# Optimization experiments

Hardware: AMD Instinct MI355X
Metric: run time of the kernel (lower is better)

The kernel has to match this reference:

```python
import jax, jax.numpy as jnp
import numpy as np

N = 100000
E = 1600000
DIM = 128
HID = 16
HEADS = 4
NUM_CLASSES = 2
NEG_SLOPE = 0.2


def _glorot(key, shape):
    fan_in, fan_out = shape[0], shape[-1]
    lim = jnp.sqrt(6.0 / (fan_in + fan_out))
    return jax.random.uniform(key, shape, jnp.float32, -lim, lim)


def setup_inputs() -> dict:
    key = jax.random.key(0)
    ks = jax.random.split(key, 12)
    x = jax.random.normal(ks[0], (N, DIM), jnp.float32)
    edge_index = jax.random.randint(ks[1], (2, E), 0, N, jnp.int32)
    # conv1: in=DIM, out=HID, heads=HEADS
    W1 = _glorot(ks[2], (DIM, HEADS * HID))
    att_src1 = _glorot(ks[3], (HEADS, HID))
    att_dst1 = _glorot(ks[4], (HEADS, HID))
    b1 = jnp.zeros((HEADS * HID,), jnp.float32)
    # conv2: in=HEADS*HID, out=NUM_CLASSES, heads=1
    W2 = _glorot(ks[5], (HEADS * HID, NUM_CLASSES))
    att_src2 = _glorot(ks[6], (1, NUM_CLASSES))
    att_dst2 = _glorot(ks[7], (1, NUM_CLASSES))
    b2 = jnp.zeros((NUM_CLASSES,), jnp.float32)
    return {"x": x, "edge_index": edge_index, "W1": W1, "att_src1": att_src1,
            "att_dst1": att_dst1, "b1": b1, "W2": W2, "att_src2": att_src2,
            "att_dst2": att_dst2, "b2": b2}


def gat_conv(x, src, dst, W, a_src, a_dst, bias, heads, out_ch):
    n = x.shape[0]
    h = (x @ W).reshape(n, heads, out_ch)                      # [N,H,C]
    alpha_s = jnp.sum(h * a_src[None], axis=-1)                # [N,H]
    alpha_d = jnp.sum(h * a_dst[None], axis=-1)                # [N,H]
    e = alpha_s[src] + alpha_d[dst]                            # [Etot,H]
    e = jnp.where(e > 0, e, NEG_SLOPE * e)                     # leaky_relu
    m = jax.ops.segment_max(e, dst, num_segments=n)            # segment softmax
    e = jnp.exp(e - m[dst])
    s = jax.ops.segment_sum(e, dst, num_segments=n)
    alpha = e / (s[dst] + 1e-16)                               # [Etot,H]
    msg = h[src] * alpha[..., None]                            # [Etot,H,C]
    out = jax.ops.segment_sum(msg, dst, num_segments=n)        # [N,H,C]
    return out.reshape(n, heads * out_ch) + bias


def reference(x, edge_index, W1, att_src1, att_dst1, b1, W2, att_src2, att_dst2, b2):
    n = x.shape[0]
    loops = jnp.arange(n, dtype=edge_index.dtype)
    src = jnp.concatenate([edge_index[0], loops])
    dst = jnp.concatenate([edge_index[1], loops])
    # dropout p=0.6 is identity in eval mode
    h = gat_conv(x, src, dst, W1, att_src1, att_dst1, b1, HEADS, HID)
    h = jax.nn.elu(h)
    out = gat_conv(h, src, dst, W2, att_src2, att_dst2, b2, 1, NUM_CLASSES)
    return out
```

## Files before the change

### kernel.cpp

```cpp
#include <hip/hip_runtime.h>
#include <math.h>


#define NB 256
#define BSH 9
#define SRC_MASK 0x1FFFF
#define KC_CHUNK 2048
#define KC_PT 8
#define MAXB 9216

static __device__ __forceinline__ unsigned short f2bf(float f) {
    union { float f; unsigned int u; } v; v.f = f;
    unsigned int r = (v.u + 0x7fffu + ((v.u >> 16) & 1u)) >> 16;
    return (unsigned short)r;
}
static __device__ __forceinline__ float bf2f(unsigned short s) {
    union { unsigned int u; float f; } v; v.u = ((unsigned int)s) << 16;
    return v.f;
}
static __device__ __forceinline__ float lrexp(float raw) {
    return __expf(raw > 0.f ? raw : 0.2f * raw);
}

__global__ __launch_bounds__(256) void k_gemm1(const float* __restrict__ x,
                                               const float* __restrict__ W,
                                               const float* __restrict__ att_s,
                                               const float* __restrict__ att_d,
                                               unsigned short* __restrict__ h1b,
                                               float* __restrict__ as1,
                                               float* __restrict__ ad1,
                                               int* __restrict__ bcursor, int n) {
    __shared__ float xs[64 * 132];
    __shared__ float Ws[128 * 64];
    const int t = threadIdx.x;
    const int row0 = blockIdx.x * 64;
    if (blockIdx.x == 0) bcursor[t] = 0;
    for (int i = t; i < 2048; i += 256)
        ((float4*)Ws)[i] = ((const float4*)W)[i];
    for (int i = t; i < 2048; i += 256) {
        int r = i >> 5, k4 = i & 31;
        float4 v = make_float4(0.f, 0.f, 0.f, 0.f);
        if (row0 + r < n) v = ((const float4*)x)[(size_t)(row0 + r) * 32 + k4];
        *(float4*)&xs[r * 132 + k4 * 4] = v;
    }
    __syncthreads();
    const int tx = t & 15, ty = t >> 4;
    float acc[4][4] = {};
    for (int k = 0; k < 128; k += 4) {
        float4 av[4], bv[4];
#pragma unroll
        for (int i = 0; i < 4; ++i) av[i] = *(const float4*)&xs[(ty * 4 + i) * 132 + k];
#pragma unroll
        for (int kk = 0; kk < 4; ++kk) bv[kk] = *(const float4*)&Ws[(k + kk) * 64 + tx * 4];
#pragma unroll
        for (int kk = 0; kk < 4; ++kk) {
            float4 b = bv[kk];
#pragma unroll
            for (int i = 0; i < 4; ++i) {
                float a = ((const float*)&av[i])[kk];
                acc[i][0] += a * b.x; acc[i][1] += a * b.y;
                acc[i][2] += a * b.z; acc[i][3] += a * b.w;
            }
        }
    }
    float4 sv = ((const float4*)att_s)[tx];
    float4 dv = ((const float4*)att_d)[tx];
    float ps[4], pd[4];
#pragma unroll
    for (int i = 0; i < 4; ++i) {
        ps[i] = acc[i][0] * sv.x + acc[i][1] * sv.y + acc[i][2] * sv.z + acc[i][3] * sv.w;
        pd[i] = acc[i][0] * dv.x + acc[i][1] * dv.y + acc[i][2] * dv.z + acc[i][3] * dv.w;
        int r = row0 + ty * 4 + i;
        if (r < n) {
            ushort4 b;
            b.x = f2bf(acc[i][0]); b.y = f2bf(acc[i][1]);
            b.z = f2bf(acc[i][2]); b.w = f2bf(acc[i][3]);
            ((ushort4*)h1b)[(size_t)r * 16 + tx] = b;
        }
    }
    __syncthreads();
    float* redA = xs;
    float* redB = xs + 1024;
#pragma unroll
    for (int i = 0; i < 4; ++i) {
        int row = ty * 4 + i;
        redA[row * 16 + tx] = ps[i];
        redB[row * 16 + tx] = pd[i];
    }
    __syncthreads();
    {
        int row = t >> 2, h = t & 3;
        int r = row0 + row;
        if (r < n) {
            const float* pa = &redA[row * 16 + h * 4];
            const float* pb = &redB[row * 16 + h * 4];
            as1[r * 4 + h] = pa[0] + pa[1] + pa[2] + pa[3];
            ad1[r * 4 + h] = pb[0] + pb[1] + pb[2] + pb[3];
        }
    }
}

__global__ __launch_bounds__(256) void kC_bin(const int* __restrict__ src,
                                              const int* __restrict__ dst,
                                              int* __restrict__ bcursor,
                                              unsigned int* __restrict__ staged, int E) {
    __shared__ unsigned int pairs[KC_CHUNK];
    __shared__ unsigned char binOf[KC_CHUNK];
    __shared__ int h[NB], lofs[NB], lcur[NB], gbase[NB];
    int t = threadIdx.x;
    int base = blockIdx.x * KC_CHUNK;
    int cnt = E - base; if (cnt > KC_CHUNK) cnt = KC_CHUNK;
    h[t] = 0; __syncthreads();
    unsigned int myV[KC_PT]; int myBin[KC_PT];
#pragma unroll
    for (int k = 0; k < KC_PT; ++k) {
        int li = k * 256 + t;
        myBin[k] = -1;
        if (li < cnt) {
            int gi = base + li;
            int s = src[gi], d = dst[gi];
            int bin = d >> BSH;
            myV[k] = ((unsigned int)(d & ((1 << BSH) - 1)) << 17) | (unsigned int)s;
            myBin[k] = bin;
            atomicAdd(&h[bin], 1);
        }
    }
    __syncthreads();
    int hv = h[t];
    lofs[t] = hv; __syncthreads();
    for (int o = 1; o < NB; o <<= 1) {
        int xv = (t >= o) ? lofs[t - o] : 0;
        __syncthreads();
        lofs[t] += xv; __syncthreads();
    }
    int excl = lofs[t] - hv;
    if (hv) gbase[t] = t * MAXB + atomicAdd(&bcursor[t], hv);
    __syncthreads();
    lofs[t] = excl; lcur[t] = excl;
    __syncthreads();
#pragma unroll
    for (int k = 0; k < KC_PT; ++k) {
        if (myBin[k] >= 0) {
            int p = atomicAdd(&lcur[myBin[k]], 1);
            pairs[p] = myV[k];
            binOf[p] = (unsigned char)myBin[k];
        }
    }
    __syncthreads();
    for (int i = t; i < cnt; i += 256) {
        int b = binOf[i];
        staged[gbase[b] + (i - lofs[b])] = pairs[i];
    }
}

__global__ __launch_bounds__(256) void kD_group(const unsigned int* __restrict__ staged,
                                                const int* __restrict__ bcursor,
                                                unsigned int* __restrict__ grouped,
                                                int* __restrict__ offs,
                                                int* __restrict__ dcnt, int n) {
    __shared__ int lh[512], lofs2[512], lcur2[512];
    __shared__ unsigned int st[MAXB];
    int t = threadIdx.x;
    int b = blockIdx.x;
    int base = b * MAXB;
    int cnt = bcursor[b];
    lh[t] = 0; lh[t + 256] = 0;
    __syncthreads();
    for (int i = t; i < cnt; i += 256)
        atomicAdd(&lh[staged[base + i] >> 17], 1);
    __syncthreads();
    int a0 = lh[2 * t], a1 = lh[2 * t + 1];
    int sp = a0 + a1;
    lcur2[t] = sp; __syncthreads();
    for (int o = 1; o < NB; o <<= 1) {
        int xv = (t >= o) ? lcur2[t - o] : 0;
        __syncthreads();
        lcur2[t] += xv; __syncthreads();
    }
    int excl = lcur2[t] - sp;
    lofs2[2 * t] = excl; lofs2[2 * t + 1] = excl + a0;
    __syncthreads();
#pragma unroll
    for (int q = 0; q < 2; ++q) {
        int dl = t + q * 256;
        int d = (b << BSH) + dl;
        if (d < n) {
            offs[d] = base + lofs2[dl];
            dcnt[d] = lh[dl];
        }
        lcur2[dl] = lofs2[dl];
    }
    __syncthreads();
    for (int i = t; i < cnt; i += 256) {
        unsigned int v = staged[base + i];
        int p = atomicAdd(&lcur2[v >> 17], 1);
        st[p] = v;
    }
    __syncthreads();
    for (int i = t; i < cnt; i += 256)
        grouped[base + i] = st[i];
}

__global__ __launch_bounds__(256) void k_agg1(
        const int* __restrict__ offs, const int* __restrict__ dcnt,
        const unsigned int* __restrict__ grouped,
        const unsigned short* __restrict__ h1b, const float* __restrict__ as1,
        const float* __restrict__ ad1, const float* __restrict__ b1,
        const float* __restrict__ W2,
        const float* __restrict__ att_s2, const float* __restrict__ att_d2,
        float4* __restrict__ pack, int n) {
    const int lane = threadIdx.x & 63;
    const int d = blockIdx.x * 4 + (threadIdx.x >> 6);
    if (d >= n) return;
    const int c = lane;
    const int h = lane >> 4;
    const int sub = lane & 15;
    const int off0 = offs[d];
    const int total = dcnt[d];
    const float adh = ad1[d * 4 + h];
    const float wselfv = lrexp(as1[d * 4 + h] + adh);

    float acc = wselfv * bf2f(h1b[(size_t)d * 64 + c]);
    float wsum = 0.f;

    int s_cur = d; float a_cur = 0.f; bool v_ok = (sub < total);
    if (v_ok) {
        unsigned int v = grouped[off0 + sub];
        s_cur = (int)(v & SRC_MASK);
        a_cur = as1[s_cur * 4 + h];
    }
    for (int base = 0; base < total; base += 16) {
        int en = base + 16 + sub;
        bool n_ok = (en < total);
        unsigned int v_n = 0;
        if (n_ok) v_n = grouped[off0 + en];

        float w = v_ok ? lrexp(a_cur + adh) : 0.f;
        wsum += w;
        int s = s_cur;
#pragma unroll
        for (int j = 0; j < 16; ++j) {
            int sj = __builtin_amdgcn_readlane(s, j);
            float wj = __shfl(w, (h << 4) + j);
            acc += wj * bf2f(h1b[(size_t)sj * 64 + c]);
        }
        int s_n = d; float a_n = 0.f;
        if (n_ok) {
            s_n = (int)(v_n & SRC_MASK);
            a_n = as1[s_n * 4 + h];
        }
        s_cur = s_n; a_cur = a_n; v_ok = n_ok;
    }
    wsum += __shfl_xor(wsum, 1);
    wsum += __shfl_xor(wsum, 2);
    wsum += __shfl_xor(wsum, 4);
    wsum += __shfl_xor(wsum, 8);
    wsum += wselfv;
    float o1 = acc / (wsum + 1e-16f) + b1[c];
    float o = o1 > 0.f ? o1 : (__expf(o1) - 1.f);
    float2 wv = ((const float2*)W2)[c];
    float p0 = o * wv.x, p1 = o * wv.y;
#pragma unroll
    for (int m = 1; m < 64; m <<= 1) {
        p0 += __shfl_xor(p0, m);
        p1 += __shfl_xor(p1, m);
    }
    if (lane == 0) {
        pack[d] = make_float4(p0, p1,
                              p0 * att_s2[0] + p1 * att_s2[1],
                              p0 * att_d2[0] + p1 * att_d2[1]);
    }
}

__global__ __launch_bounds__(256) void k_agg2(
        const int* __restrict__ offs, const int* __restrict__ dcnt,
        const unsigned int* __restrict__ grouped,
        const float4* __restrict__ pack, const float* __restrict__ b2,
        float* __restrict__ out, int n) {
    int t = threadIdx.x;
    int g = blockIdx.x * 16 + (t >> 4);
    int sub = t & 15;
    if (g >= n) return;
    int off0 = offs[g];
    int total = dcnt[g];
    float4 pg = pack[g];
    float ad = pg.w;
    float a0 = 0.f, a1 = 0.f, ws = 0.f;
    if (sub == 0) {
        float w = lrexp(pg.z + ad);
        a0 = w * pg.x; a1 = w * pg.y; ws = w;
    }
    for (int e = sub; e < total; e += 16) {
        int s = (int)(grouped[off0 + e] & SRC_MASK);
        float4 ps = pack[s];
        float w = lrexp(ps.z + ad);
        a0 += w * ps.x; a1 += w * ps.y; ws += w;
    }
#pragma unroll
    for (int m = 1; m < 16; m <<= 1) {
        a0 += __shfl_xor(a0, m);
        a1 += __shfl_xor(a1, m);
        ws += __shfl_xor(ws, m);
    }
    if (sub == 0) {
        float inv = 1.f / (ws + 1e-16f);
        out[(size_t)g * 2 + 0] = a0 * inv + b2[0];
        out[(size_t)g * 2 + 1] = a1 * inv + b2[1];
    }
}

extern "C" void kernel_launch(void* const* d_in, const int* in_sizes, int n_in,
                              void* d_out, int out_size, void* d_ws, size_t ws_size,
                              hipStream_t stream) {
    const float* x    = (const float*)d_in[0];
    const int*   ei   = (const int*)d_in[1];
    const float* W1   = (const float*)d_in[2];
    const float* as1w = (const float*)d_in[3];
    const float* ad1w = (const float*)d_in[4];
    const float* b1   = (const float*)d_in[5];
    const float* W2   = (const float*)d_in[6];
    const float* as2w = (const float*)d_in[7];
    const float* ad2w = (const float*)d_in[8];
    const float* b2   = (const float*)d_in[9];
    const int n = in_sizes[0] / 128;
    const int E = in_sizes[1] / 2;
    float* out = (float*)d_out;

    char* ws = (char*)d_ws;
    size_t off = 0;
    auto alloc = [&](size_t bytes) {
        void* p = ws + off;
        off = (off + bytes + 255) & ~(size_t)255;
        return p;
    };
    unsigned short* h1b = (unsigned short*)alloc((size_t)n * 64 * 2);
    float*  as1    = (float*)alloc((size_t)n * 4 * 4);
    float*  ad1    = (float*)alloc((size_t)n * 4 * 4);
    float4* pack   = (float4*)alloc((size_t)n * 16);
    int*    offs   = (int*)alloc((size_t)n * 4);
    int*    dcnt   = (int*)alloc((size_t)n * 4);
    int*    bcursor= (int*)alloc(NB * 4);
    unsigned int* staged  = (unsigned int*)alloc((size_t)NB * MAXB * 4);
    unsigned int* grouped = (unsigned int*)alloc((size_t)NB * MAXB * 4);

    const int nblk = (E + KC_CHUNK - 1) / KC_CHUNK;
    const int nbk = (n + 511) >> 9;
    k_gemm1<<<(n + 63) / 64, 256, 0, stream>>>(x, W1, as1w, ad1w, h1b, as1, ad1,
                                               bcursor, n);
    kC_bin<<<nblk, 256, 0, stream>>>(ei, ei + E, bcursor, staged, E);
    kD_group<<<nbk, 256, 0, stream>>>(staged, bcursor, grouped, offs, dcnt, n);
    k_agg1<<<(n + 3) / 4, 256, 0, stream>>>(offs, dcnt, grouped, h1b, as1, ad1,
                                            b1, W2, as2w, ad2w, pack, n);
    k_agg2<<<(n + 15) / 16, 256, 0, stream>>>(offs, dcnt, grouped, pack, b2, out, n);
}
```

Before: 241.0 us.

## Fuse GEMM and edge binning into one launch; per-lane row gather in agg1

Merges the layer-1 GEMM and the edge-binning pass into a single kernel whose blocks branch on blockIdx, and zeroes the bin cursors with a memset, so the two independent stages can overlap on the GPU. In k_agg1 each lane now loads a whole 16-element bf16 slice of one source row (two uint4 loads) and keeps 16 partial accumulators. A butterfly shuffle transpose then reduces these to per-channel values, replacing the 16-step readlane/shfl loop. The fused kernel uses a larger shared allocation (about 65 KB), which may reduce occupancy for the binning blocks.

```diff
diff --git a/kernel.cpp b/kernel.cpp
--- a/kernel.cpp
+++ b/kernel.cpp
@@ -14,142 +14,138 @@
     unsigned int r = (v.u + 0x7fffu + ((v.u >> 16) & 1u)) >> 16;
     return (unsigned short)r;
 }
-static __device__ __forceinline__ float bf2f(unsigned short s) {
-    union { unsigned int u; float f; } v; v.u = ((unsigned int)s) << 16;
-    return v.f;
-}
 static __device__ __forceinline__ float lrexp(float raw) {
     return __expf(raw > 0.f ? raw : 0.2f * raw);
 }
 
-__global__ __launch_bounds__(256) void k_gemm1(const float* __restrict__ x,
-                                               const float* __restrict__ W,
-                                               const float* __restrict__ att_s,
-                                               const float* __restrict__ att_d,
-                                               unsigned short* __restrict__ h1b,
-                                               float* __restrict__ as1,
-                                               float* __restrict__ ad1,
-                                               int* __restrict__ bcursor, int n) {
-    __shared__ float xs[64 * 132];
-    __shared__ float Ws[128 * 64];
+__global__ __launch_bounds__(256) void k_gemm_bin(
+        const float* __restrict__ x, const float* __restrict__ W,
+        const float* __restrict__ att_s, const float* __restrict__ att_d,
+        unsigned short* __restrict__ h1b, float* __restrict__ as1,
+        float* __restrict__ ad1,
+        const int* __restrict__ esrc, const int* __restrict__ edst,
+        int* __restrict__ bcursor, unsigned int* __restrict__ staged,
+        int nG, int E, int n) {
+    __shared__ __align__(16) char smem[66560];
     const int t = threadIdx.x;
-    const int row0 = blockIdx.x * 64;
-    if (blockIdx.x == 0) bcursor[t] = 0;
-    for (int i = t; i < 2048; i += 256)
-        ((float4*)Ws)[i] = ((const float4*)W)[i];
-    for (int i = t; i < 2048; i += 256) {
-        int r = i >> 5, k4 = i & 31;
-        float4 v = make_float4(0.f, 0.f, 0.f, 0.f);
-        if (row0 + r < n) v = ((const float4*)x)[(size_t)(row0 + r) * 32 + k4];
-        *(float4*)&xs[r * 132 + k4 * 4] = v;
-    }
-    __syncthreads();
-    const int tx = t & 15, ty = t >> 4;
-    float acc[4][4] = {};
-    for (int k = 0; k < 128; k += 4) {
-        float4 av[4], bv[4];
-#pragma unroll
-        for (int i = 0; i < 4; ++i) av[i] = *(const float4*)&xs[(ty * 4 + i) * 132 + k];
-#pragma unroll
-        for (int kk = 0; kk < 4; ++kk) bv[kk] = *(const float4*)&Ws[(k + kk) * 64 + tx * 4];
-#pragma unroll
-        for (int kk = 0; kk < 4; ++kk) {
-            float4 b = bv[kk];
-#pragma unroll
-            for (int i = 0; i < 4; ++i) {
-                float a = ((const float*)&av[i])[kk];
-                acc[i][0] += a * b.x; acc[i][1] += a * b.y;
-                acc[i][2] += a * b.z; acc[i][3] += a * b.w;
+
+    if (blockIdx.x < nG) {
+        float* xs = (float*)smem;
+        float* Ws = (float*)(smem + 33792);
+        const int row0 = blockIdx.x * 64;
+        for (int i = t; i < 2048; i += 256)
+            ((float4*)Ws)[i] = ((const float4*)W)[i];
+        for (int i = t; i < 2048; i += 256) {
+            int r = i >> 5, k4 = i & 31;
+            float4 v = make_float4(0.f, 0.f, 0.f, 0.f);
+            if (row0 + r < n) v = ((const float4*)x)[(size_t)(row0 + r) * 32 + k4];
+            *(float4*)&xs[r * 132 + k4 * 4] = v;
+        }
+        __syncthreads();
+        const int tx = t & 15, ty = t >> 4;
+        float acc[4][4] = {};
+        for (int k = 0; k < 128; k += 4) {
+            float4 av[4], bv[4];
+#pragma unroll
+            for (int i = 0; i < 4; ++i) av[i] = *(const float4*)&xs[(ty * 4 + i) * 132 + k];
+#pragma unroll
+            for (int kk = 0; kk < 4; ++kk) bv[kk] = *(const float4*)&Ws[(k + kk) * 64 + tx * 4];
+#pragma unroll
+            for (int kk = 0; kk < 4; ++kk) {
+                float4 b = bv[kk];
+#pragma unroll
+                for (int i = 0; i < 4; ++i) {
+                    float a = ((const float*)&av[i])[kk];
+                    acc[i][0] += a * b.x; acc[i][1] += a * b.y;
+                    acc[i][2] += a * b.z; acc[i][3] += a * b.w;
+                }
             }
         }
-    }
-    float4 sv = ((const float4*)att_s)[tx];
-    float4 dv = ((const float4*)att_d)[tx];
-    float ps[4], pd[4];
-#pragma unroll
-    for (int i = 0; i < 4; ++i) {
-        ps[i] = acc[i][0] * sv.x + acc[i][1] * sv.y + acc[i][2] * sv.z + acc[i][3] * sv.w;
-        pd[i] = acc[i][0] * dv.x + acc[i][1] * dv.y + acc[i][2] * dv.z + acc[i][3] * dv.w;
-        int r = row0 + ty * 4 + i;
-        if (r < n) {
-            ushort4 b;
-            b.x = f2bf(acc[i][0]); b.y = f2bf(acc[i][1]);
-            b.z = f2bf(acc[i][2]); b.w = f2bf(acc[i][3]);
-            ((ushort4*)h1b)[(size_t)r * 16 + tx] = b;
-        }
-    }
-    __syncthreads();
-    float* redA = xs;
-    float* redB = xs + 1024;
-#pragma unroll
-    for (int i = 0; i < 4; ++i) {
-        int row = ty * 4 + i;
-        redA[row * 16 + tx] = ps[i];
-        redB[row * 16 + tx] = pd[i];
-    }
-    __syncthreads();
-    {
-        int row = t >> 2, h = t & 3;
-        int r = row0 + row;
-        if (r < n) {
-            const float* pa = &redA[row * 16 + h * 4];
-            const float* pb = &redB[row * 16 + h * 4];
-            as1[r * 4 + h] = pa[0] + pa[1] + pa[2] + pa[3];
-            ad1[r * 4 + h] = pb[0] + pb[1] + pb[2] + pb[3];
-        }
-    }
-}
-
-__global__ __launch_bounds__(256) void kC_bin(const int* __restrict__ src,
-                                              const int* __restrict__ dst,
-                                              int* __restrict__ bcursor,
-                                              unsigned int* __restrict__ staged, int E) {
-    __shared__ unsigned int pairs[KC_CHUNK];
-    __shared__ unsigned char binOf[KC_CHUNK];
-    __shared__ int h[NB], lofs[NB], lcur[NB], gbase[NB];
-    int t = threadIdx.x;
-    int base = blockIdx.x * KC_CHUNK;
-    int cnt = E - base; if (cnt > KC_CHUNK) cnt = KC_CHUNK;
-    h[t] = 0; __syncthreads();
-    unsigned int myV[KC_PT]; int myBin[KC_PT];
-#pragma unroll
-    for (int k = 0; k < KC_PT; ++k) {
-        int li = k * 256 + t;
-        myBin[k] = -1;
-        if (li < cnt) {
-            int gi = base + li;
-            int s = src[gi], d = dst[gi];
-            int bin = d >> BSH;
-            myV[k] = ((unsigned int)(d & ((1 << BSH) - 1)) << 17) | (unsigned int)s;
-            myBin[k] = bin;
-            atomicAdd(&h[bin], 1);
-        }
-    }
-    __syncthreads();
-    int hv = h[t];
-    lofs[t] = hv; __syncthreads();
-    for (int o = 1; o < NB; o <<= 1) {
-        int xv = (t >= o) ? lofs[t - o] : 0;
-        __syncthreads();
-        lofs[t] += xv; __syncthreads();
-    }
-    int excl = lofs[t] - hv;
-    if (hv) gbase[t] = t * MAXB + atomicAdd(&bcursor[t], hv);
-    __syncthreads();
-    lofs[t] = excl; lcur[t] = excl;
-    __syncthreads();
-#pragma unroll
-    for (int k = 0; k < KC_PT; ++k) {
-        if (myBin[k] >= 0) {
-            int p = atomicAdd(&lcur[myBin[k]], 1);
-            pairs[p] = myV[k];
-            binOf[p] = (unsigned char)myBin[k];
-        }
-    }
-    __syncthreads();
-    for (int i = t; i < cnt; i += 256) {
-        int b = binOf[i];
-        staged[gbase[b] + (i - lofs[b])] = pairs[i];
+        float4 sv = ((const float4*)att_s)[tx];
+        float4 dv = ((const float4*)att_d)[tx];
+        float ps[4], pd[4];
+#pragma unroll
+        for (int i = 0; i < 4; ++i) {
+            ps[i] = acc[i][0] * sv.x + acc[i][1] * sv.y + acc[i][2] * sv.z + acc[i][3] * sv.w;
+            pd[i] = acc[i][0] * dv.x + acc[i][1] * dv.y + acc[i][2] * dv.z + acc[i][3] * dv.w;
+            int r = row0 + ty * 4 + i;
+            if (r < n) {
+                ushort4 b;
+                b.x = f2bf(acc[i][0]); b.y = f2bf(acc[i][1]);
+                b.z = f2bf(acc[i][2]); b.w = f2bf(acc[i][3]);
+                ((ushort4*)h1b)[(size_t)r * 16 + tx] = b;
+            }
+        }
+        __syncthreads();
+        float* redA = xs;
+        float* redB = xs + 1024;
+#pragma unroll
+        for (int i = 0; i < 4; ++i) {
+            int row = ty * 4 + i;
+            redA[row * 16 + tx] = ps[i];
+            redB[row * 16 + tx] = pd[i];
+        }
+        __syncthreads();
+        {
+            int row = t >> 2, h = t & 3;
+            int r = row0 + row;
+            if (r < n) {
+                const float* pa = &redA[row * 16 + h * 4];
+                const float* pb = &redB[row * 16 + h * 4];
+                as1[r * 4 + h] = pa[0] + pa[1] + pa[2] + pa[3];
+                ad1[r * 4 + h] = pb[0] + pb[1] + pb[2] + pb[3];
+            }
+        }
+    } else {
+        unsigned int* pairs = (unsigned int*)smem;
+        unsigned char* binOf = (unsigned char*)(smem + 8192);
+        int* hh    = (int*)(smem + 10240);
+        int* lofs  = (int*)(smem + 11264);
+        int* lcur  = (int*)(smem + 12288);
+        int* gbase = (int*)(smem + 13312);
+        int base = (blockIdx.x - nG) * KC_CHUNK;
+        int cnt = E - base; if (cnt > KC_CHUNK) cnt = KC_CHUNK;
+        hh[t] = 0; __syncthreads();
+        unsigned int myV[KC_PT]; int myBin[KC_PT];
+#pragma unroll
+        for (int k = 0; k < KC_PT; ++k) {
+            int li = k * 256 + t;
+            myBin[k] = -1;
+            if (li < cnt) {
+                int gi = base + li;
+                int s = esrc[gi], d = edst[gi];
+                int bin = d >> BSH;
+                myV[k] = ((unsigned int)(d & ((1 << BSH) - 1)) << 17) | (unsigned int)s;
+                myBin[k] = bin;
+                atomicAdd(&hh[bin], 1);
+            }
+        }
+        __syncthreads();
+        int hv = hh[t];
+        lofs[t] = hv; __syncthreads();
+        for (int o = 1; o < NB; o <<= 1) {
+            int xv = (t >= o) ? lofs[t - o] : 0;
+            __syncthreads();
+            lofs[t] += xv; __syncthreads();
+        }
+        int excl = lofs[t] - hv;
+        if (hv) gbase[t] = t * MAXB + atomicAdd(&bcursor[t], hv);
+        __syncthreads();
+        lofs[t] = excl; lcur[t] = excl;
+        __syncthreads();
+#pragma unroll
+        for (int k = 0; k < KC_PT; ++k) {
+            if (myBin[k] >= 0) {
+                int p = atomicAdd(&lcur[myBin[k]], 1);
+                pairs[p] = myV[k];
+                binOf[p] = (unsigned char)myBin[k];
+            }
+        }
+        __syncthreads();
+        for (int i = t; i < cnt; i += 256) {
+            int b = binOf[i];
+            staged[gbase[b] + (i - lofs[b])] = pairs[i];
+        }
     }
 }
 
@@ -212,53 +208,100 @@
     const int lane = threadIdx.x & 63;
     const int d = blockIdx.x * 4 + (threadIdx.x >> 6);
     if (d >= n) return;
-    const int c = lane;
-    const int h = lane >> 4;
+    const int q = lane >> 4;
     const int sub = lane & 15;
     const int off0 = offs[d];
     const int total = dcnt[d];
-    const float adh = ad1[d * 4 + h];
-    const float wselfv = lrexp(as1[d * 4 + h] + adh);
-
-    float acc = wselfv * bf2f(h1b[(size_t)d * 64 + c]);
+    const float adh = ad1[d * 4 + q];
+    const float wselfv = lrexp(as1[d * 4 + q] + adh);
+
+    float acc[16];
+#pragma unroll
+    for (int k = 0; k < 16; ++k) acc[k] = 0.f;
     float wsum = 0.f;
+
+    if (sub == 0) {
+        const uint4* rp = (const uint4*)(h1b + (size_t)d * 64 + q * 16);
+        uint4 ra = rp[0], rb = rp[1];
+        const unsigned int* ua = (const unsigned int*)&ra;
+        const unsigned int* ub = (const unsigned int*)&rb;
+#pragma unroll
+        for (int j = 0; j < 4; ++j) {
+            acc[2 * j]     += wselfv * __uint_as_float(ua[j] << 16);
+            acc[2 * j + 1] += wselfv * __uint_as_float(ua[j] & 0xffff0000u);
+            acc[8 + 2 * j] += wselfv * __uint_as_float(ub[j] << 16);
+            acc[9 + 2 * j] += wselfv * __uint_as_float(ub[j] & 0xffff0000u);
+        }
+    }
 
     int s_cur = d; float a_cur = 0.f; bool v_ok = (sub < total);
     if (v_ok) {
         unsigned int v = grouped[off0 + sub];
         s_cur = (int)(v & SRC_MASK);
-        a_cur = as1[s_cur * 4 + h];
+        a_cur = as1[s_cur * 4 + q];
     }
     for (int base = 0; base < total; base += 16) {
+        const uint4* rp = (const uint4*)(h1b + (size_t)s_cur * 64 + q * 16);
+        uint4 ra = rp[0], rb = rp[1];
         int en = base + 16 + sub;
         bool n_ok = (en < total);
         unsigned int v_n = 0;
         if (n_ok) v_n = grouped[off0 + en];
-
         float w = v_ok ? lrexp(a_cur + adh) : 0.f;
         wsum += w;
-        int s = s_cur;
-#pragma unroll
-        for (int j = 0; j < 16; ++j) {
-            int sj = __builtin_amdgcn_readlane(s, j);
-            float wj = __shfl(w, (h << 4) + j);
-            acc += wj * bf2f(h1b[(size_t)sj * 64 + c]);
-        }
         int s_n = d; float a_n = 0.f;
         if (n_ok) {
             s_n = (int)(v_n & SRC_MASK);
-            a_n = as1[s_n * 4 + h];
+            a_n = as1[s_n * 4 + q];
+        }
+        const unsigned int* ua = (const unsigned int*)&ra;
+        const unsigned int* ub = (const unsigned int*)&rb;
+#pragma unroll
+        for (int j = 0; j < 4; ++j) {
+            acc[2 * j]     += w * __uint_as_float(ua[j] << 16);
+            acc[2 * j + 1] += w * __uint_as_float(ua[j] & 0xffff0000u);
+            acc[8 + 2 * j] += w * __uint_as_float(ub[j] << 16);
+            acc[9 + 2 * j] += w * __uint_as_float(ub[j] & 0xffff0000u);
         }
         s_cur = s_n; a_cur = a_n; v_ok = n_ok;
     }
+
     wsum += __shfl_xor(wsum, 1);
     wsum += __shfl_xor(wsum, 2);
     wsum += __shfl_xor(wsum, 4);
     wsum += __shfl_xor(wsum, 8);
     wsum += wselfv;
-    float o1 = acc / (wsum + 1e-16f) + b1[c];
+
+    float v8[8];
+    {
+        int b0 = sub & 1;
+#pragma unroll
+        for (int k = 0; k < 8; ++k)
+            v8[k] = acc[2 * k + b0] + __shfl_xor(acc[2 * k + (b0 ^ 1)], 1);
+    }
+    float v4[4];
+    {
+        int b = (sub >> 1) & 1;
+#pragma unroll
+        for (int k = 0; k < 4; ++k)
+            v4[k] = v8[2 * k + b] + __shfl_xor(v8[2 * k + (b ^ 1)], 2);
+    }
+    float v2[2];
+    {
+        int b = (sub >> 2) & 1;
+#pragma unroll
+        for (int k = 0; k < 2; ++k)
+            v2[k] = v4[2 * k + b] + __shfl_xor(v4[2 * k + (b ^ 1)], 4);
+    }
+    float vfin;
+    {
+        int b = (sub >> 3) & 1;
+        vfin = v2[b] + __shfl_xor(v2[b ^ 1], 8);
+    }
+
+    float o1 = vfin / (wsum + 1e-16f) + b1[lane];
     float o = o1 > 0.f ? o1 : (__expf(o1) - 1.f);
-    float2 wv = ((const float2*)W2)[c];
+    float2 wv = ((const float2*)W2)[lane];
     float p0 = o * wv.x, p1 = o * wv.y;
 #pragma unroll
     for (int m = 1; m < 64; m <<= 1) {
@@ -343,11 +386,13 @@
     unsigned int* staged  = (unsigned int*)alloc((size_t)NB * MAXB * 4);
     unsigned int* grouped = (unsigned int*)alloc((size_t)NB * MAXB * 4);
 
-    const int nblk = (E + KC_CHUNK - 1) / KC_CHUNK;
+    hipMemsetAsync(bcursor, 0, NB * 4, stream);
+
+    const int nG = (n + 63) / 64;
+    const int nB = (E + KC_CHUNK - 1) / KC_CHUNK;
     const int nbk = (n + 511) >> 9;
-    k_gemm1<<<(n + 63) / 64, 256, 0, stream>>>(x, W1, as1w, ad1w, h1b, as1, ad1,
-                                               bcursor, n);
-    kC_bin<<<nblk, 256, 0, stream>>>(ei, ei + E, bcursor, staged, E);
+    k_gemm_bin<<<nG + nB, 256, 0, stream>>>(x, W1, as1w, ad1w, h1b, as1, ad1,
+                                            ei, ei + E, bcursor, staged, nG, E, n);
     kD_group<<<nbk, 256, 0, stream>>>(staged, bcursor, grouped, offs, dcnt, n);
     k_agg1<<<(n + 3) / 4, 256, 0, stream>>>(offs, dcnt, grouped, h1b, as1, ad1,
                                             b1, W2, as2w, ad2w, pack, n);
```

Result: slower. 299.9 us (+24.5%).
